# Optimization experiments

Measured on AMD Instinct MI355X. Metric: run time of the kernel, lower is better.

Reference implementation:

```python
import jax, jax.numpy as jnp
import numpy as np

D_EMBED = 64
N_HEADS = 4
D_HEAD = D_EMBED // N_HEADS
D_FF = 96          # int(1.5 * d_embed)
D_MODEL = 128      # repeat_factor = d_model // d_embed = 2
EPS = 1e-5
B = 4
# (idx_start, kernel_size, channels_in, kernel_no) per layer of the source CNN
LAYERS = [(0, 9, 8, 256), (18688, 9, 16, 256), (55808, 9, 16, 512)]
N_PARAMS = 130048
MAX_SEQ = max(ks * cin for _, ks, cin, _ in LAYERS) + 1  # 145


def _kernel_indices(start, ks, cin, kno):
    # Static ragged slice indices: per kernel, its weights plus trailing bias.
    L = ks * cin
    base = start + np.arange(kno)[:, None] * L + np.arange(L)[None, :]
    bias = start + kno * L + np.arange(kno)
    return np.concatenate([base, bias[:, None]], axis=1)  # (kno, L+1)


_IDX = [jnp.asarray(_kernel_indices(*l)) for l in LAYERS]


def setup_inputs():
    key = jax.random.key(0)
    k = jax.random.split(key, 8)
    s = 1.0 / np.sqrt(D_EMBED)
    return {
        "x": jax.random.normal(k[0], (B, N_PARAMS), dtype=jnp.float32),
        "pos_emb": jax.random.normal(k[1], (MAX_SEQ, D_EMBED), dtype=jnp.float32) * s,
        "comp_token": jax.random.normal(k[2], (D_EMBED,), dtype=jnp.float32),
        "in_proj_w": jax.random.normal(k[3], (3 * D_EMBED, D_EMBED), dtype=jnp.float32) * s,
        "in_proj_b": jnp.zeros((3 * D_EMBED,), jnp.float32),
        "out_proj_w": jax.random.normal(k[4], (D_EMBED, D_EMBED), dtype=jnp.float32) * s,
        "out_proj_b": jnp.zeros((D_EMBED,), jnp.float32),
        "lin1_w": jax.random.normal(k[5], (D_FF, D_EMBED), dtype=jnp.float32) * s,
        "lin1_b": jnp.zeros((D_FF,), jnp.float32),
        "lin2_w": jax.random.normal(k[6], (D_EMBED, D_FF), dtype=jnp.float32) / np.sqrt(D_FF),
        "lin2_b": jnp.zeros((D_EMBED,), jnp.float32),
        "ln1_w": jnp.ones((D_EMBED,), jnp.float32),
        "ln1_b": jnp.zeros((D_EMBED,), jnp.float32),
        "ln2_w": jnp.ones((D_EMBED,), jnp.float32),
        "ln2_b": jnp.zeros((D_EMBED,), jnp.float32),
    }


def _layernorm(x, w, b):
    mu = jnp.mean(x, axis=-1, keepdims=True)
    var = jnp.mean(jnp.square(x - mu), axis=-1, keepdims=True)
    return (x - mu) * jax.lax.rsqrt(var + EPS) * w + b


def _encoder(t, in_proj_w, in_proj_b, out_proj_w, out_proj_b,
             lin1_w, lin1_b, lin2_w, lin2_b, ln1_w, ln1_b, ln2_w, ln2_b):
    # Post-norm TransformerEncoderLayer (relu, eval mode -> dropout = identity).
    M, S, _ = t.shape
    qkv = t @ in_proj_w.T + in_proj_b                     # (M, S, 3D)
    q, k, v = jnp.split(qkv, 3, axis=-1)
    heads = lambda u: u.reshape(M, S, N_HEADS, D_HEAD).transpose(0, 2, 1, 3)
    q, k, v = heads(q), heads(k), heads(v)
    attn = jax.nn.softmax(jnp.einsum('mhsd,mhtd->mhst', q, k) / np.sqrt(D_HEAD))
    o = jnp.einsum('mhst,mhtd->mhsd', attn, v).transpose(0, 2, 1, 3).reshape(M, S, D_EMBED)
    o = o @ out_proj_w.T + out_proj_b
    h = _layernorm(t + o, ln1_w, ln1_b)
    ff = jax.nn.relu(h @ lin1_w.T + lin1_b) @ lin2_w.T + lin2_b
    return _layernorm(h + ff, ln2_w, ln2_b)


def reference(x, pos_emb, comp_token, in_proj_w, in_proj_b, out_proj_w, out_proj_b,
              lin1_w, lin1_b, lin2_w, lin2_b, ln1_w, ln1_b, ln2_w, ln2_b):
    enc = (in_proj_w, in_proj_b, out_proj_w, out_proj_b,
           lin1_w, lin1_b, lin2_w, lin2_b, ln1_w, ln1_b, ln2_w, ln2_b)
    outs = []
    for idx in _IDX:  # fixed small loop over layers; kernels within a layer are batched
        K, n = idx.shape
        w = x[:, idx]                                     # (B, K, n) ragged gather
        tok = w[..., None] + pos_emb[:n]                  # scalar -> d_embed broadcast + pos add
        cls = jnp.broadcast_to(comp_token, (B, K, 1, D_EMBED))
        tok = jnp.concatenate([cls, tok], axis=2).reshape(B * K, n + 1, D_EMBED)
        y = _encoder(tok, *enc)[:, 0, :]                  # comp-token readout
        outs.append(y.reshape(B, K, D_EMBED))
    y = jnp.concatenate(outs, axis=1)                     # (B, 1024, d_embed)
    return jnp.tile(y, (1, 1, D_MODEL // D_EMBED))        # (B, 1024, d_model)
```

## Files before the change

kernel.cpp:

```cpp
#include <hip/hip_runtime.h>
#include <math.h>

#define NPAR 130048
#define EPSF 1e-5f

typedef _Float16 hfp;
typedef _Float16 h2x __attribute__((ext_vector_type(2)));
typedef _Float16 h4x __attribute__((ext_vector_type(4)));
typedef float    f4x __attribute__((ext_vector_type(4)));

#define BSTR  164
#define VSTR2 172
#define ATSTR 172
#define WOSTR 76
#define L2STRH 108

#define OFF_VPOST 0
#define OFF_WO    5504
#define OFF_L1    7936
#define OFF_L2    11584
#define OFF_BETA  15040
#define OFF_SM    15696
#define SM_CT   0
#define SM_BO   64
#define SM_B1   128
#define SM_B2   224
#define SM_LN1W 288
#define SM_LN1B 352
#define SM_LN2W 416
#define SM_LN2B 480
#define SM_ALPH 544
#define SM_GAM  548
#define SM_BOCT 576

#define L_W    0
#define L_WB   2304
#define L_ATT  2320
#define L_INVS 7824
#define L_O    7888
#define L_H1   8496
#define L_R    9104
#define L_PRE  9968
#define L_RED  11056
#define LDS_FLOATS 11072

template<int C>
__device__ __forceinline__ float dppf(float x) {
    return __int_as_float(__builtin_amdgcn_update_dpp(0, __float_as_int(x), C, 0xf, 0xf, false));
}
__device__ __forceinline__ float rowsum16(float x) {
    x += dppf<0x128>(x); x += dppf<0x124>(x); x += dppf<0x122>(x); x += dppf<0x121>(x);
    return x;
}
__device__ __forceinline__ unsigned packh2(float a, float b) {
    union { h2x h; unsigned u; } cv;
    cv.h.x = (hfp)a; cv.h.y = (hfp)b;
    return cv.u;
}

__global__ __launch_bounds__(64) void k_pre(const float* __restrict__ pe,
                                            const float* __restrict__ ct,
                                            const float* __restrict__ W,
                                            const float* __restrict__ bq,
                                            const float* __restrict__ Wo,
                                            const float* __restrict__ bo,
                                            const float* __restrict__ L1w,
                                            const float* __restrict__ b1,
                                            const float* __restrict__ L2w,
                                            const float* __restrict__ b2,
                                            const float* __restrict__ ln1w,
                                            const float* __restrict__ ln1b,
                                            const float* __restrict__ ln2w,
                                            const float* __restrict__ ln2b,
                                            float* __restrict__ ws)
{
    const int j = blockIdx.x;
    const int o = threadIdx.x;
    hfp* wsh = (hfp*)ws;

    if (j < 145) {
        const float4* wq4 = (const float4*)(W + o*64);
        const float4* wk4 = (const float4*)(W + (64 + o)*64);
        const float4* wv4 = (const float4*)(W + (128 + o)*64);
        const float4* p4  = (const float4*)(pe + j*64);
        float sk = bq[64 + o], sv = bq[128 + o], sq = bq[o];
        #pragma unroll
        for (int e = 0; e < 16; ++e) {
            float4 k4 = wk4[e], v4 = wv4[e], q4 = wq4[e], pp = p4[e];
            float4 cc = ((const float4*)ct)[e];
            sk += k4.x*pp.x + k4.y*pp.y + k4.z*pp.z + k4.w*pp.w;
            sv += v4.x*pp.x + v4.y*pp.y + v4.z*pp.z + v4.w*pp.w;
            sq += q4.x*cc.x + q4.y*cc.y + q4.z*cc.z + q4.w*cc.w;
        }
        wsh[o*VSTR2 + j] = (hfp)sv;
        float r = sq * sk;
        #pragma unroll
        for (int off = 1; off < 16; off <<= 1) r += __shfl_xor(r, off);
        if ((o & 15) == 0) ws[OFF_BETA + (o >> 4)*BSTR + j] = r;
    } else if (j == 145) {
        const float4* wq4 = (const float4*)(W + o*64);
        const float4* wk4 = (const float4*)(W + (64 + o)*64);
        const float4* wv4 = (const float4*)(W + (128 + o)*64);
        float sq = bq[o], sk = bq[64 + o], sv = bq[128 + o], suk = 0.f, suv = 0.f;
        #pragma unroll
        for (int e = 0; e < 16; ++e) {
            float4 k4 = wk4[e], v4 = wv4[e], q4 = wq4[e];
            float4 cc = ((const float4*)ct)[e];
            sq += q4.x*cc.x + q4.y*cc.y + q4.z*cc.z + q4.w*cc.w;
            sk += k4.x*cc.x + k4.y*cc.y + k4.z*cc.z + k4.w*cc.w;
            sv += v4.x*cc.x + v4.y*cc.y + v4.z*cc.z + v4.w*cc.w;
            suk += k4.x + k4.y + k4.z + k4.w;
            suv += v4.x + v4.y + v4.z + v4.w;
        }
        wsh[o*VSTR2 + 156] = (hfp)sv;
        wsh[o*VSTR2 + 157] = (hfp)suv;
        #pragma unroll
        for (int c = 145; c < 156; ++c) wsh[o*VSTR2 + c] = (hfp)0.f;
        wsh[o*VSTR2 + 158] = (hfp)0.f;
        wsh[o*VSTR2 + 159] = (hfp)0.f;
        float a = sq * suk, g = sq * sk;
        #pragma unroll
        for (int off = 1; off < 16; off <<= 1) {
            a += __shfl_xor(a, off);
            g += __shfl_xor(g, off);
        }
        if ((o & 15) == 0) {
            ws[OFF_SM + SM_ALPH + (o >> 4)] = a;
            ws[OFF_SM + SM_GAM  + (o >> 4)] = g;
        }
    } else if (j == 146) {
        ws[OFF_SM + SM_CT   + o] = ct[o];
        ws[OFF_SM + SM_BO   + o] = bo[o];
        ws[OFF_SM + SM_BOCT + o] = bo[o] + ct[o];
        ws[OFF_SM + SM_B2   + o] = b2[o];
        ws[OFF_SM + SM_LN1W + o] = ln1w[o];
        ws[OFF_SM + SM_LN1B + o] = ln1b[o];
        ws[OFF_SM + SM_LN2W + o] = ln2w[o];
        ws[OFF_SM + SM_LN2B + o] = ln2b[o];
        ws[OFF_SM + SM_B1   + o] = b1[o];
        if (o < 32) ws[OFF_SM + SM_B1 + 64 + o] = b1[64 + o];
    } else if (j == 147) {
        for (int idx = o; idx < 4096; idx += 64)
            wsh[OFF_WO*2 + (idx >> 6)*WOSTR + (idx & 63)] = (hfp)Wo[idx];
    } else if (j == 148) {
        for (int idx = o; idx < 6144; idx += 64)
            wsh[OFF_L1*2 + (idx >> 6)*WOSTR + (idx & 63)] = (hfp)L1w[idx];
    } else {
        for (int idx = o; idx < 6144; idx += 64) {
            int r = idx / 96, c = idx - r*96;
            wsh[OFF_L2*2 + r*L2STRH + c] = (hfp)L2w[idx];
        }
    }
}

template<int L>
__device__ __forceinline__ void run_group(const float* __restrict__ x,
                                          const float* __restrict__ ws,
                                          float* __restrict__ lds,
                                          float* __restrict__ out,
                                          int b, int k0, int start, int kno, int kgo)
{
    const int tid  = threadIdx.x;
    const int wave = tid >> 6;
    const int lane = tid & 63;
    const int e16  = lane & 15;
    const int g4   = (lane >> 4) * 4;
    const int c0   = e16 * 4;
    const hfp* wsh  = (const hfp*)ws;
    const hfp* ldsh = (const hfp*)lds;

    float wm = 0.f;
    {
        const f4x* src = (const f4x*)(x + (size_t)b*NPAR + start + (size_t)k0*L);
        f4x* dst = (f4x*)(lds + L_W);
        #pragma unroll
        for (int c = 0; c < (4*L + 255)/256; ++c) {
            int i4 = c*256 + tid;
            if (i4 < 4*L) {
                f4x v = src[i4];
                dst[i4] = v;
                wm = fmaxf(wm, fmaxf(fmaxf(fabsf(v.x), fabsf(v.y)), fmaxf(fabsf(v.z), fabsf(v.w))));
            }
        }
        if (tid < 16) {
            float bwv = x[(size_t)b*NPAR + start + (size_t)kno*L + k0 + tid];
            lds[L_WB + tid] = bwv;
            wm = fmaxf(wm, fabsf(bwv));
        }
    }

    h4x vpf[10];
    #pragma unroll
    for (int kt = 0; kt < 10; ++kt)
        vpf[kt] = *(const h4x*)(wsh + (16*wave + e16)*VSTR2 + kt*16 + g4);
    h4x wof[4];
    #pragma unroll
    for (int kt = 0; kt < 4; ++kt)
        wof[kt] = *(const h4x*)(wsh + OFF_WO*2 + (16*wave + e16)*WOSTR + kt*16 + g4);
    h4x l1f[2][4];
    float b1v[2];
    #pragma unroll
    for (int u = 0; u < 2; ++u) {
        const int tt = wave + 4*u;
        if (tt < 6) {
            #pragma unroll
            for (int kt = 0; kt < 4; ++kt)
                l1f[u][kt] = *(const h4x*)(wsh + OFF_L1*2 + (16*tt + e16)*WOSTR + kt*16 + g4);
            b1v[u] = ws[OFF_SM + SM_B1 + 16*tt + e16];
        }
    }
    h4x l2f[6];
    #pragma unroll
    for (int kt = 0; kt < 6; ++kt)
        l2f[kt] = *(const h4x*)(wsh + OFF_L2*2 + (16*wave + e16)*L2STRH + kt*16 + g4);
    const int nw = 16*wave + e16;
    const float boct = ws[OFF_SM + SM_BOCT + nw];
    const float b2v  = ws[OFF_SM + SM_B2   + nw];
    const int hsm = (tid >> 2) & 3;
    const float alpha = ws[OFF_SM + SM_ALPH + hsm];
    const float gam   = ws[OFF_SM + SM_GAM  + hsm];
    const f4x ln1w4 = *(const f4x*)(ws + OFF_SM + SM_LN1W + c0);
    const f4x ln1b4 = *(const f4x*)(ws + OFF_SM + SM_LN1B + c0);
    const f4x ln2w4 = *(const f4x*)(ws + OFF_SM + SM_LN2W + c0);
    const f4x ln2b4 = *(const f4x*)(ws + OFF_SM + SM_LN2B + c0);

    {
        #pragma unroll
        for (int off = 1; off < 64; off <<= 1) wm = fmaxf(wm, __shfl_xor(wm, off));
        if (lane == 0) lds[L_RED + wave] = wm;
        float mb = -1e30f;
        for (int j = lane; j < 145; j += 64) mb = fmaxf(mb, ws[OFF_BETA + wave*BSTR + j]);
        #pragma unroll
        for (int off = 1; off < 64; off <<= 1) mb = fmaxf(mb, __shfl_xor(mb, off));
        if (lane == 0) lds[L_RED + 8 + wave] = mb;
    }
    __syncthreads();

    {
        const float wmax = fmaxf(fmaxf(lds[L_RED+0], lds[L_RED+1]),
                                 fmaxf(lds[L_RED+2], lds[L_RED+3]));
        const int r = tid >> 2;
        const int m = r >> 2, h = r & 3, q = tid & 3;
        const float mbh = lds[L_RED + 8 + h];
        const float M = fmaxf(0.25f*(fabsf(alpha)*wmax + mbh), 0.25f*gam);
        unsigned* arow32 = (unsigned*)(lds + L_ATT) + r*(ATSTR/2);
        const float* wr = lds + L_W + m*L;
        const float* br = ws + OFF_BETA + h*BSTR;
        float S = 0.f, WS = 0.f;
        #pragma unroll
        for (int t = 0; t < 10; ++t) {
            const int j0 = 16*t + 4*q;
            if (16*t + 15 < L || j0 + 3 < L) {
                f4x wv = *(const f4x*)(wr + j0);
                f4x bv = *(const f4x*)(br + j0);
                float p0 = __expf(fmaf(alpha, wv.x, bv.x)*0.25f - M);
                float p1 = __expf(fmaf(alpha, wv.y, bv.y)*0.25f - M);
                float p2 = __expf(fmaf(alpha, wv.z, bv.z)*0.25f - M);
                float p3 = __expf(fmaf(alpha, wv.w, bv.w)*0.25f - M);
                S  += (p0 + p1) + (p2 + p3);
                WS += (p0*wv.x + p1*wv.y) + (p2*wv.z + p3*wv.w);
                uint2 u; u.x = packh2(p0, p1); u.y = packh2(p2, p3);
                *(uint2*)(arow32 + (j0 >> 1)) = u;
            } else if (j0 <= L) {
                float pv4[4] = {0.f, 0.f, 0.f, 0.f};
                #pragma unroll
                for (int ee = 0; ee < 4; ++ee) {
                    int j = j0 + ee;
                    if (j <= L) {
                        float w = (j < L) ? wr[j] : lds[L_WB + m];
                        float p = __expf(fmaf(alpha, w, br[j])*0.25f - M);
                        S += p; WS += p*w; pv4[ee] = p;
                    }
                }
                uint2 u; u.x = packh2(pv4[0], pv4[1]); u.y = packh2(pv4[2], pv4[3]);
                *(uint2*)(arow32 + (j0 >> 1)) = u;
            } else if (j0 != 156) {
                uint2 z; z.x = 0u; z.y = 0u;
                *(uint2*)(arow32 + (j0 >> 1)) = z;
            }
        }
        S  += __shfl_xor(S, 1);  S  += __shfl_xor(S, 2);
        WS += __shfl_xor(WS, 1); WS += __shfl_xor(WS, 2);
        const float pc = __expf(0.25f*gam - M);
        S += pc;
        if (q == 0) {
            lds[L_INVS + r] = 1.f / S;
            arow32[78] = packh2(pc, WS);
            arow32[79] = 0u;
        }
    }
    __syncthreads();

    {
        const hfp* atth = ldsh + L_ATT*2;
        const int hh = wave;
        f4x vacc = (f4x){0.f,0.f,0.f,0.f};
        #pragma unroll
        for (int kt = 0; kt < 10; ++kt) {
            h4x a = *(const h4x*)(atth + (e16*4 + hh)*ATSTR + kt*16 + g4);
            vacc = __builtin_amdgcn_mfma_f32_16x16x16f16(a, vpf[kt], vacc, 0, 0, 0);
        }
        hfp* Oh = (hfp*)(lds + L_O);
        #pragma unroll
        for (int rr = 0; rr < 4; ++rr) {
            float sc = lds[L_INVS + (g4 + rr)*4 + hh];
            Oh[(g4 + rr)*WOSTR + 16*hh + e16] = (hfp)(vacc[rr] * sc);
        }
    }
    __syncthreads();

    {
        const hfp* Oh = ldsh + L_O*2;
        f4x pacc = (f4x){0.f,0.f,0.f,0.f};
        #pragma unroll
        for (int kt = 0; kt < 4; ++kt) {
            h4x a = *(const h4x*)(Oh + e16*WOSTR + kt*16 + g4);
            pacc = __builtin_amdgcn_mfma_f32_16x16x16f16(a, wof[kt], pacc, 0, 0, 0);
        }
        #pragma unroll
        for (int rr = 0; rr < 4; ++rr)
            lds[L_PRE + (g4 + rr)*68 + nw] = pacc[rr] + boct;
    }
    __syncthreads();

    {
        const int m = wave*4 + (lane >> 4);
        f4x pv = *(const f4x*)(lds + L_PRE + m*68 + c0);
        float s = (pv.x + pv.y) + (pv.z + pv.w);
        float mu = rowsum16(s) * (1.f/64.f);
        f4x d; d.x = pv.x-mu; d.y = pv.y-mu; d.z = pv.z-mu; d.w = pv.w-mu;
        float v = (d.x*d.x + d.y*d.y) + (d.z*d.z + d.w*d.w);
        float rs = rsqrtf(rowsum16(v)*(1.f/64.f) + EPSF);
        h4x hv;
        hv.x = (hfp)(d.x*rs*ln1w4.x + ln1b4.x);
        hv.y = (hfp)(d.y*rs*ln1w4.y + ln1b4.y);
        hv.z = (hfp)(d.z*rs*ln1w4.z + ln1b4.z);
        hv.w = (hfp)(d.w*rs*ln1w4.w + ln1b4.w);
        *(h4x*)((hfp*)(lds + L_H1) + m*WOSTR + c0) = hv;
    }
    __syncthreads();

    {
        const hfp* H1h = ldsh + L_H1*2;
        h4x af[4];
        #pragma unroll
        for (int kt = 0; kt < 4; ++kt) af[kt] = *(const h4x*)(H1h + e16*WOSTR + kt*16 + g4);
        hfp* Rh = (hfp*)(lds + L_R);
        #pragma unroll
        for (int u = 0; u < 2; ++u) {
            const int tt = wave + 4*u;
            if (tt < 6) {
                f4x racc = (f4x){0.f,0.f,0.f,0.f};
                #pragma unroll
                for (int kt = 0; kt < 4; ++kt)
                    racc = __builtin_amdgcn_mfma_f32_16x16x16f16(af[kt], l1f[u][kt], racc, 0, 0, 0);
                const int n = 16*tt + e16;
                #pragma unroll
                for (int rr = 0; rr < 4; ++rr)
                    Rh[(g4 + rr)*L2STRH + n] = (hfp)fmaxf(racc[rr] + b1v[u], 0.f);
            }
        }
    }
    __syncthreads();

    {
        const hfp* Rh2 = ldsh + L_R*2;
        f4x yacc = (f4x){0.f,0.f,0.f,0.f};
        #pragma unroll
        for (int kt = 0; kt < 6; ++kt) {
            h4x a = *(const h4x*)(Rh2 + e16*L2STRH + kt*16 + g4);
            yacc = __builtin_amdgcn_mfma_f32_16x16x16f16(a, l2f[kt], yacc, 0, 0, 0);
        }
        #pragma unroll
        for (int rr = 0; rr < 4; ++rr)
            lds[L_PRE + (g4 + rr)*68 + nw] = yacc[rr] + b2v;
    }
    __syncthreads();

    {
        const int m = wave*4 + (lane >> 4);
        f4x pv = *(const f4x*)(lds + L_PRE + m*68 + c0);
        h4x h1p = *(const h4x*)((const hfp*)(lds + L_H1) + m*WOSTR + c0);
        f4x tot;
        tot.x = pv.x + (float)h1p.x;
        tot.y = pv.y + (float)h1p.y;
        tot.z = pv.z + (float)h1p.z;
        tot.w = pv.w + (float)h1p.w;
        float s = (tot.x + tot.y) + (tot.z + tot.w);
        float mu = rowsum16(s) * (1.f/64.f);
        f4x d; d.x = tot.x-mu; d.y = tot.y-mu; d.z = tot.z-mu; d.w = tot.w-mu;
        float v = (d.x*d.x + d.y*d.y) + (d.z*d.z + d.w*d.w);
        float rs = rsqrtf(rowsum16(v)*(1.f/64.f) + EPSF);
        f4x y;
        y.x = d.x*rs*ln2w4.x + ln2b4.x;
        y.y = d.y*rs*ln2w4.y + ln2b4.y;
        y.z = d.z*rs*ln2w4.z + ln2b4.z;
        y.w = d.w*rs*ln2w4.w + ln2b4.w;
        float* ob = out + ((size_t)b*1024 + kgo + k0 + m)*128;
        *(f4x*)(ob + c0)      = y;
        *(f4x*)(ob + 64 + c0) = y;
    }
}

__global__ __launch_bounds__(256, 1) void k_main(const float* __restrict__ x,
                                                 const float* __restrict__ ws,
                                                 float* __restrict__ out)
{
    __shared__ __align__(16) float lds[LDS_FLOATS];
    const int w = blockIdx.x;
    if (w < 64) {
        run_group<72>(x, ws, lds, out, w >> 4, (w & 15)*16, 0, 256, 0);
    } else if (w < 128) {
        const int w2 = w - 64;
        run_group<144>(x, ws, lds, out, w2 >> 4, (w2 & 15)*16, 18688, 256, 256);
    } else {
        const int w3 = w - 128;
        run_group<144>(x, ws, lds, out, w3 >> 5, (w3 & 31)*16, 55808, 512, 512);
    }
}

extern "C" void kernel_launch(void* const* d_in, const int* in_sizes, int n_in,
                              void* d_out, int out_size, void* d_ws, size_t ws_size,
                              hipStream_t stream) {
    const float* x    = (const float*)d_in[0];
    const float* pe   = (const float*)d_in[1];
    const float* ct   = (const float*)d_in[2];
    const float* Wq   = (const float*)d_in[3];
    const float* bq   = (const float*)d_in[4];
    const float* Wo   = (const float*)d_in[5];
    const float* bo   = (const float*)d_in[6];
    const float* L1w  = (const float*)d_in[7];
    const float* b1   = (const float*)d_in[8];
    const float* L2w  = (const float*)d_in[9];
    const float* b2   = (const float*)d_in[10];
    const float* ln1w = (const float*)d_in[11];
    const float* ln1b = (const float*)d_in[12];
    const float* ln2w = (const float*)d_in[13];
    const float* ln2b = (const float*)d_in[14];
    float* out = (float*)d_out;
    float* ws  = (float*)d_ws;

    k_pre <<<150, 64, 0, stream>>>(pe, ct, Wq, bq, Wo, bo, L1w, b1, L2w, b2,
                                   ln1w, ln1b, ln2w, ln2b, ws);
    k_main<<<256, 256, 0, stream>>>(x, ws, out);
}
```

Baseline: 19.40 us.

## Halve kernels per block to 8, use exact per-row softmax max, double grid

Each block now handles 8 kernels instead of 16, so the grid doubles to 512 blocks and LDS use is halved, allowing two blocks per CU through the launch bounds. The softmax stabilizer is no longer a block-wide bound built from a cross-wave max reduction and an extra barrier. Each row now computes its exact max with an 8-lane shuffle reduction. The 16-row MFMA tiles now carry only 8 valid rows, so half the matrix work is wasted, and the max step adds a second pass over the inputs.

```diff
diff --git a/kernel.cpp b/kernel.cpp
--- a/kernel.cpp
+++ b/kernel.cpp
@@ -34,15 +34,14 @@
 #define SM_BOCT 576
 
 #define L_W    0
-#define L_WB   2304
-#define L_ATT  2320
-#define L_INVS 7824
-#define L_O    7888
-#define L_H1   8496
-#define L_R    9104
-#define L_PRE  9968
-#define L_RED  11056
-#define LDS_FLOATS 11072
+#define L_WB   1152
+#define L_ATT  1168
+#define L_INVS 3920
+#define L_O    3952
+#define L_H1   4256
+#define L_R    4560
+#define L_PRE  4992
+#define LDS_FLOATS 5536
 
 template<int C>
 __device__ __forceinline__ float dppf(float x) {
@@ -164,29 +163,21 @@
     const int wave = tid >> 6;
     const int lane = tid & 63;
     const int e16  = lane & 15;
+    const int e8   = e16 & 7;
     const int g4   = (lane >> 4) * 4;
     const int c0   = e16 * 4;
     const hfp* wsh  = (const hfp*)ws;
     const hfp* ldsh = (const hfp*)lds;
 
-    float wm = 0.f;
     {
         const f4x* src = (const f4x*)(x + (size_t)b*NPAR + start + (size_t)k0*L);
         f4x* dst = (f4x*)(lds + L_W);
         #pragma unroll
-        for (int c = 0; c < (4*L + 255)/256; ++c) {
+        for (int c = 0; c < (2*L + 255)/256; ++c) {
             int i4 = c*256 + tid;
-            if (i4 < 4*L) {
-                f4x v = src[i4];
-                dst[i4] = v;
-                wm = fmaxf(wm, fmaxf(fmaxf(fabsf(v.x), fabsf(v.y)), fmaxf(fabsf(v.z), fabsf(v.w))));
-            }
-        }
-        if (tid < 16) {
-            float bwv = x[(size_t)b*NPAR + start + (size_t)kno*L + k0 + tid];
-            lds[L_WB + tid] = bwv;
-            wm = fmaxf(wm, fabsf(bwv));
-        }
+            if (i4 < 2*L) dst[i4] = src[i4];
+        }
+        if (tid < 8) lds[L_WB + tid] = x[(size_t)b*NPAR + start + (size_t)kno*L + k0 + tid];
     }
 
     h4x vpf[10];
@@ -216,41 +207,54 @@
     const int nw = 16*wave + e16;
     const float boct = ws[OFF_SM + SM_BOCT + nw];
     const float b2v  = ws[OFF_SM + SM_B2   + nw];
-    const int hsm = (tid >> 2) & 3;
-    const float alpha = ws[OFF_SM + SM_ALPH + hsm];
-    const float gam   = ws[OFF_SM + SM_GAM  + hsm];
     const f4x ln1w4 = *(const f4x*)(ws + OFF_SM + SM_LN1W + c0);
     const f4x ln1b4 = *(const f4x*)(ws + OFF_SM + SM_LN1B + c0);
     const f4x ln2w4 = *(const f4x*)(ws + OFF_SM + SM_LN2W + c0);
     const f4x ln2b4 = *(const f4x*)(ws + OFF_SM + SM_LN2B + c0);
-
-    {
-        #pragma unroll
-        for (int off = 1; off < 64; off <<= 1) wm = fmaxf(wm, __shfl_xor(wm, off));
-        if (lane == 0) lds[L_RED + wave] = wm;
-        float mb = -1e30f;
-        for (int j = lane; j < 145; j += 64) mb = fmaxf(mb, ws[OFF_BETA + wave*BSTR + j]);
-        #pragma unroll
-        for (int off = 1; off < 64; off <<= 1) mb = fmaxf(mb, __shfl_xor(mb, off));
-        if (lane == 0) lds[L_RED + 8 + wave] = mb;
-    }
-    __syncthreads();
-
-    {
-        const float wmax = fmaxf(fmaxf(lds[L_RED+0], lds[L_RED+1]),
-                                 fmaxf(lds[L_RED+2], lds[L_RED+3]));
-        const int r = tid >> 2;
-        const int m = r >> 2, h = r & 3, q = tid & 3;
-        const float mbh = lds[L_RED + 8 + h];
-        const float M = fmaxf(0.25f*(fabsf(alpha)*wmax + mbh), 0.25f*gam);
-        unsigned* arow32 = (unsigned*)(lds + L_ATT) + r*(ATSTR/2);
+    __syncthreads();
+
+    {
+        const int r = tid >> 3;
+        const int m = r >> 2, h = r & 3, q = tid & 7;
+        const float alpha = ws[OFF_SM + SM_ALPH + h];
+        const float gam   = ws[OFF_SM + SM_GAM  + h];
         const float* wr = lds + L_W + m*L;
         const float* br = ws + OFF_BETA + h*BSTR;
+        const float wbias = lds[L_WB + m];
+
+        float mx = 0.25f * gam;
+        #pragma unroll
+        for (int t = 0; t < 5; ++t) {
+            const int j0 = 32*t + 4*q;
+            if (j0 + 3 < L) {
+                f4x wv = *(const f4x*)(wr + j0);
+                f4x bv = *(const f4x*)(br + j0);
+                mx = fmaxf(mx, fmaf(alpha, wv.x, bv.x)*0.25f);
+                mx = fmaxf(mx, fmaf(alpha, wv.y, bv.y)*0.25f);
+                mx = fmaxf(mx, fmaf(alpha, wv.z, bv.z)*0.25f);
+                mx = fmaxf(mx, fmaf(alpha, wv.w, bv.w)*0.25f);
+            } else if (j0 <= L) {
+                #pragma unroll
+                for (int ee = 0; ee < 4; ++ee) {
+                    int j = j0 + ee;
+                    if (j <= L) {
+                        float w = (j < L) ? wr[j] : wbias;
+                        mx = fmaxf(mx, fmaf(alpha, w, br[j])*0.25f);
+                    }
+                }
+            }
+        }
+        mx = fmaxf(mx, __shfl_xor(mx, 1));
+        mx = fmaxf(mx, __shfl_xor(mx, 2));
+        mx = fmaxf(mx, __shfl_xor(mx, 4));
+        const float M = mx;
+
+        unsigned* arow32 = (unsigned*)(lds + L_ATT) + r*(ATSTR/2);
         float S = 0.f, WS = 0.f;
         #pragma unroll
-        for (int t = 0; t < 10; ++t) {
-            const int j0 = 16*t + 4*q;
-            if (16*t + 15 < L || j0 + 3 < L) {
+        for (int t = 0; t < 5; ++t) {
+            const int j0 = 32*t + 4*q;
+            if (j0 + 3 < L) {
                 f4x wv = *(const f4x*)(wr + j0);
                 f4x bv = *(const f4x*)(br + j0);
                 float p0 = __expf(fmaf(alpha, wv.x, bv.x)*0.25f - M);
@@ -267,7 +271,7 @@
                 for (int ee = 0; ee < 4; ++ee) {
                     int j = j0 + ee;
                     if (j <= L) {
-                        float w = (j < L) ? wr[j] : lds[L_WB + m];
+                        float w = (j < L) ? wr[j] : wbias;
                         float p = __expf(fmaf(alpha, w, br[j])*0.25f - M);
                         S += p; WS += p*w; pv4[ee] = p;
                     }
@@ -279,8 +283,8 @@
                 *(uint2*)(arow32 + (j0 >> 1)) = z;
             }
         }
-        S  += __shfl_xor(S, 1);  S  += __shfl_xor(S, 2);
-        WS += __shfl_xor(WS, 1); WS += __shfl_xor(WS, 2);
+        S  += __shfl_xor(S, 1);  S  += __shfl_xor(S, 2);  S  += __shfl_xor(S, 4);
+        WS += __shfl_xor(WS, 1); WS += __shfl_xor(WS, 2); WS += __shfl_xor(WS, 4);
         const float pc = __expf(0.25f*gam - M);
         S += pc;
         if (q == 0) {
@@ -297,14 +301,15 @@
         f4x vacc = (f4x){0.f,0.f,0.f,0.f};
         #pragma unroll
         for (int kt = 0; kt < 10; ++kt) {
-            h4x a = *(const h4x*)(atth + (e16*4 + hh)*ATSTR + kt*16 + g4);
+            h4x a = *(const h4x*)(atth + (e8*4 + hh)*ATSTR + kt*16 + g4);
             vacc = __builtin_amdgcn_mfma_f32_16x16x16f16(a, vpf[kt], vacc, 0, 0, 0);
         }
         hfp* Oh = (hfp*)(lds + L_O);
         #pragma unroll
         for (int rr = 0; rr < 4; ++rr) {
-            float sc = lds[L_INVS + (g4 + rr)*4 + hh];
-            Oh[(g4 + rr)*WOSTR + 16*hh + e16] = (hfp)(vacc[rr] * sc);
+            const int mrow = g4 + rr;
+            if (mrow < 8)
+                Oh[mrow*WOSTR + 16*hh + e16] = (hfp)(vacc[rr] * lds[L_INVS + mrow*4 + hh]);
         }
     }
     __syncthreads();
@@ -314,29 +319,33 @@
         f4x pacc = (f4x){0.f,0.f,0.f,0.f};
         #pragma unroll
         for (int kt = 0; kt < 4; ++kt) {
-            h4x a = *(const h4x*)(Oh + e16*WOSTR + kt*16 + g4);
+            h4x a = *(const h4x*)(Oh + e8*WOSTR + kt*16 + g4);
             pacc = __builtin_amdgcn_mfma_f32_16x16x16f16(a, wof[kt], pacc, 0, 0, 0);
         }
         #pragma unroll
-        for (int rr = 0; rr < 4; ++rr)
-            lds[L_PRE + (g4 + rr)*68 + nw] = pacc[rr] + boct;
+        for (int rr = 0; rr < 4; ++rr) {
+            const int mrow = g4 + rr;
+            if (mrow < 8) lds[L_PRE + mrow*68 + nw] = pacc[rr] + boct;
+        }
     }
     __syncthreads();
 
     {
         const int m = wave*4 + (lane >> 4);
-        f4x pv = *(const f4x*)(lds + L_PRE + m*68 + c0);
-        float s = (pv.x + pv.y) + (pv.z + pv.w);
-        float mu = rowsum16(s) * (1.f/64.f);
-        f4x d; d.x = pv.x-mu; d.y = pv.y-mu; d.z = pv.z-mu; d.w = pv.w-mu;
-        float v = (d.x*d.x + d.y*d.y) + (d.z*d.z + d.w*d.w);
-        float rs = rsqrtf(rowsum16(v)*(1.f/64.f) + EPSF);
-        h4x hv;
-        hv.x = (hfp)(d.x*rs*ln1w4.x + ln1b4.x);
-        hv.y = (hfp)(d.y*rs*ln1w4.y + ln1b4.y);
-        hv.z = (hfp)(d.z*rs*ln1w4.z + ln1b4.z);
-        hv.w = (hfp)(d.w*rs*ln1w4.w + ln1b4.w);
-        *(h4x*)((hfp*)(lds + L_H1) + m*WOSTR + c0) = hv;
+        if (m < 8) {
+            f4x pv = *(const f4x*)(lds + L_PRE + m*68 + c0);
+            float s = (pv.x + pv.y) + (pv.z + pv.w);
+            float mu = rowsum16(s) * (1.f/64.f);
+            f4x d; d.x = pv.x-mu; d.y = pv.y-mu; d.z = pv.z-mu; d.w = pv.w-mu;
+            float v = (d.x*d.x + d.y*d.y) + (d.z*d.z + d.w*d.w);
+            float rs = rsqrtf(rowsum16(v)*(1.f/64.f) + EPSF);
+            h4x hv;
+            hv.x = (hfp)(d.x*rs*ln1w4.x + ln1b4.x);
+            hv.y = (hfp)(d.y*rs*ln1w4.y + ln1b4.y);
+            hv.z = (hfp)(d.z*rs*ln1w4.z + ln1b4.z);
+            hv.w = (hfp)(d.w*rs*ln1w4.w + ln1b4.w);
+            *(h4x*)((hfp*)(lds + L_H1) + m*WOSTR + c0) = hv;
+        }
     }
     __syncthreads();
 
@@ -344,7 +353,7 @@
         const hfp* H1h = ldsh + L_H1*2;
         h4x af[4];
         #pragma unroll
-        for (int kt = 0; kt < 4; ++kt) af[kt] = *(const h4x*)(H1h + e16*WOSTR + kt*16 + g4);
+        for (int kt = 0; kt < 4; ++kt) af[kt] = *(const h4x*)(H1h + e8*WOSTR + kt*16 + g4);
         hfp* Rh = (hfp*)(lds + L_R);
         #pragma unroll
         for (int u = 0; u < 2; ++u) {
@@ -356,8 +365,10 @@
                     racc = __builtin_amdgcn_mfma_f32_16x16x16f16(af[kt], l1f[u][kt], racc, 0, 0, 0);
                 const int n = 16*tt + e16;
                 #pragma unroll
-                for (int rr = 0; rr < 4; ++rr)
-                    Rh[(g4 + rr)*L2STRH + n] = (hfp)fmaxf(racc[rr] + b1v[u], 0.f);
+                for (int rr = 0; rr < 4; ++rr) {
+                    const int mrow = g4 + rr;
+                    if (mrow < 8) Rh[mrow*L2STRH + n] = (hfp)fmaxf(racc[rr] + b1v[u], 0.f);
+                }
             }
         }
     }
@@ -368,54 +379,58 @@
         f4x yacc = (f4x){0.f,0.f,0.f,0.f};
         #pragma unroll
         for (int kt = 0; kt < 6; ++kt) {
-            h4x a = *(const h4x*)(Rh2 + e16*L2STRH + kt*16 + g4);
+            h4x a = *(const h4x*)(Rh2 + e8*L2STRH + kt*16 + g4);
             yacc = __builtin_amdgcn_mfma_f32_16x16x16f16(a, l2f[kt], yacc, 0, 0, 0);
         }
         #pragma unroll
-        for (int rr = 0; rr < 4; ++rr)
-            lds[L_PRE + (g4 + rr)*68 + nw] = yacc[rr] + b2v;
+        for (int rr = 0; rr < 4; ++rr) {
+            const int mrow = g4 + rr;
+            if (mrow < 8) lds[L_PRE + mrow*68 + nw] = yacc[rr] + b2v;
+        }
     }
     __syncthreads();
 
     {
         const int m = wave*4 + (lane >> 4);
-        f4x pv = *(const f4x*)(lds + L_PRE + m*68 + c0);
-        h4x h1p = *(const h4x*)((const hfp*)(lds + L_H1) + m*WOSTR + c0);
-        f4x tot;
-        tot.x = pv.x + (float)h1p.x;
-        tot.y = pv.y + (float)h1p.y;
-        tot.z = pv.z + (float)h1p.z;
-        tot.w = pv.w + (float)h1p.w;
-        float s = (tot.x + tot.y) + (tot.z + tot.w);
-        float mu = rowsum16(s) * (1.f/64.f);
-        f4x d; d.x = tot.x-mu; d.y = tot.y-mu; d.z = tot.z-mu; d.w = tot.w-mu;
-        float v = (d.x*d.x + d.y*d.y) + (d.z*d.z + d.w*d.w);
-        float rs = rsqrtf(rowsum16(v)*(1.f/64.f) + EPSF);
-        f4x y;
-        y.x = d.x*rs*ln2w4.x + ln2b4.x;
-        y.y = d.y*rs*ln2w4.y + ln2b4.y;
-        y.z = d.z*rs*ln2w4.z + ln2b4.z;
-        y.w = d.w*rs*ln2w4.w + ln2b4.w;
-        float* ob = out + ((size_t)b*1024 + kgo + k0 + m)*128;
-        *(f4x*)(ob + c0)      = y;
-        *(f4x*)(ob + 64 + c0) = y;
-    }
-}
-
-__global__ __launch_bounds__(256, 1) void k_main(const float* __restrict__ x,
+        if (m < 8) {
+            f4x pv = *(const f4x*)(lds + L_PRE + m*68 + c0);
+            h4x h1p = *(const h4x*)((const hfp*)(lds + L_H1) + m*WOSTR + c0);
+            f4x tot;
+            tot.x = pv.x + (float)h1p.x;
+            tot.y = pv.y + (float)h1p.y;
+            tot.z = pv.z + (float)h1p.z;
+            tot.w = pv.w + (float)h1p.w;
+            float s = (tot.x + tot.y) + (tot.z + tot.w);
+            float mu = rowsum16(s) * (1.f/64.f);
+            f4x d; d.x = tot.x-mu; d.y = tot.y-mu; d.z = tot.z-mu; d.w = tot.w-mu;
+            float v = (d.x*d.x + d.y*d.y) + (d.z*d.z + d.w*d.w);
+            float rs = rsqrtf(rowsum16(v)*(1.f/64.f) + EPSF);
+            f4x y;
+            y.x = d.x*rs*ln2w4.x + ln2b4.x;
+            y.y = d.y*rs*ln2w4.y + ln2b4.y;
+            y.z = d.z*rs*ln2w4.z + ln2b4.z;
+            y.w = d.w*rs*ln2w4.w + ln2b4.w;
+            float* ob = out + ((size_t)b*1024 + kgo + k0 + m)*128;
+            *(f4x*)(ob + c0)      = y;
+            *(f4x*)(ob + 64 + c0) = y;
+        }
+    }
+}
+
+__global__ __launch_bounds__(256, 2) void k_main(const float* __restrict__ x,
                                                  const float* __restrict__ ws,
                                                  float* __restrict__ out)
 {
     __shared__ __align__(16) float lds[LDS_FLOATS];
     const int w = blockIdx.x;
-    if (w < 64) {
-        run_group<72>(x, ws, lds, out, w >> 4, (w & 15)*16, 0, 256, 0);
-    } else if (w < 128) {
-        const int w2 = w - 64;
-        run_group<144>(x, ws, lds, out, w2 >> 4, (w2 & 15)*16, 18688, 256, 256);
+    if (w < 128) {
+        run_group<72>(x, ws, lds, out, w >> 5, (w & 31)*8, 0, 256, 0);
+    } else if (w < 256) {
+        const int g = w - 128;
+        run_group<144>(x, ws, lds, out, g >> 5, (g & 31)*8, 18688, 256, 256);
     } else {
-        const int w3 = w - 128;
-        run_group<144>(x, ws, lds, out, w3 >> 5, (w3 & 31)*16, 55808, 512, 512);
+        const int g = w - 256;
+        run_group<144>(x, ws, lds, out, g >> 6, (g & 63)*8, 55808, 512, 512);
     }
 }
 
@@ -442,5 +457,5 @@
 
     k_pre <<<150, 64, 0, stream>>>(pe, ct, Wq, bq, Wo, bo, L1w, b1, L2w, b2,
                                    ln1w, ln1b, ln2w, ln2b, ws);
-    k_main<<<256, 256, 0, stream>>>(x, ws, out);
-}
+    k_main<<<512, 256, 0, stream>>>(x, ws, out);
+}
```

Result: slower. 20.24 us (+4.3%).
